# Optimization experiments

Hardware: AMD Instinct MI355X
Metric: run time of the kernel (lower is better)

The kernel has to match this reference:

```python
import jax, jax.numpy as jnp
import numpy as np

Z = 100000      # batch (edges)
MUL = 16        # multiplicity of Rs_in1 / Rs_out irreps
DW = MUL * 1 * MUL  # 256 weights per path (mul_1*mul_2*mul_out)
SQRT2 = 2.0 ** 0.5
SQRT3 = 3.0 ** 0.5
COUNT0 = 32.0 ** 0.5   # l=0 output: paths (0,0,0) and (1,1,0), 16+16 contributions
COUNT1 = 48.0 ** 0.5   # l=1 output: paths (0,1,1),(1,0,1),(1,1,1), 16*3 contributions


def setup_inputs() -> dict:
    key = jax.random.key(0)
    k1, k2, k3 = jax.random.split(key, 3)
    x1 = jax.random.normal(k1, (Z, 64), dtype=jnp.float32)    # [(16,0),(16,1)]
    x2 = jax.random.normal(k2, (Z, 4), dtype=jnp.float32)     # [(1,0),(1,1)]
    w = jax.random.normal(k3, (Z, 5 * DW), dtype=jnp.float32) # 5 paths x 256
    return {"x1": x1, "x2": x2, "w": w}


def reference(x1, x2, w):
    z = x1.shape[0]
    # slice inputs into irreps
    s1_0 = x1[:, :MUL]                          # (z, 16)        l=0
    s1_1 = x1[:, MUL:MUL + 3 * MUL].reshape(z, MUL, 3)  # (z, 16, 3)  l=1
    s2_0 = x2[:, :1]                            # (z, 1)         l=0
    s2_1 = x2[:, 1:4].reshape(z, 1, 3)          # (z, 1, 3)      l=1
    # per-path weights (z, u=16, v=1, w=16)
    sw0 = w[:, 0 * DW:1 * DW].reshape(z, MUL, 1, MUL)
    sw1 = w[:, 1 * DW:2 * DW].reshape(z, MUL, 1, MUL)
    sw2 = w[:, 2 * DW:3 * DW].reshape(z, MUL, 1, MUL)
    sw3 = w[:, 3 * DW:4 * DW].reshape(z, MUL, 1, MUL) / SQRT3
    sw4 = w[:, 4 * DW:5 * DW].reshape(z, MUL, 1, MUL) / SQRT2
    out0 = jnp.einsum('zuvw,zu,zv->zw', sw0, s1_0, s2_0)
    out1 = jnp.einsum('zuvw,zu,zvi->zwi', sw1, s1_0, s2_1)
    out1 = out1 + jnp.einsum('zuvw,zui,zv->zwi', sw2, s1_1, s2_0)
    out0 = out0 + jnp.einsum('zuvw,zui,zvi->zw', sw3, s1_1, s2_1)
    cross = jnp.cross(s1_1[:, :, None, :], s2_1[:, None, :, :], axis=3)  # (z,16,1,3)
    out1 = out1 + jnp.einsum('zuvw,zuvi->zwi', sw4, cross)
    # count normalization
    out0 = out0 / COUNT0                        # (z, 16)
    out1 = (out1 / COUNT1).reshape(z, 3 * MUL)  # (z, 48)
    return jnp.concatenate([out0, out1], axis=1)  # (z, 64)
```

## Files before the change

kernel.cpp:

```cpp
#include <hip/hip_runtime.h>


__global__ __launch_bounds__(256, 4) void ctp_kernel(
    const float* __restrict__ x1,
    const float* __restrict__ x2,
    const float* __restrict__ w,
    float* __restrict__ out,
    int Z)
{
    const int lane = threadIdx.x & 63;
    const int wid  = threadIdx.x >> 6;
    const int wavesPerBlock = blockDim.x >> 6;
    const int gwave  = blockIdx.x * wavesPerBlock + wid;
    const int nwaves = gridDim.x * wavesPerBlock;

    const int u = lane >> 2;
    const int c = lane & 3;

    const float inv32 = 0.17677669529663687f;
    const float inv48 = 0.14433756729740643f;
    const float inv3  = 0.57735026918962576f;
    const float inv2  = 0.70710678118654752f;

    for (int row = gwave; row < Z; row += nwaves) {
        const float* x1r = x1 + (size_t)row * 64;
        const float4 x2v = *(const float4*)(x2 + (size_t)row * 4);
        const float s20   = x2v.x;
        const float s21_0 = x2v.y, s21_1 = x2v.z, s21_2 = x2v.w;

        const float s10   = x1r[u];
        const float s11_0 = x1r[16 + 3*u + 0];
        const float s11_1 = x1r[16 + 3*u + 1];
        const float s11_2 = x1r[16 + 3*u + 2];

        const float4* wr = (const float4*)(w + (size_t)row * 1280);
        const float4 w0 = wr[lane];
        const float4 w1 = wr[ 64 + lane];
        const float4 w2 = wr[128 + lane];
        const float4 w3 = wr[192 + lane];
        const float4 w4 = wr[256 + lane];

        const float ka  = s10 * s20 * inv32;
        const float kd  = (s11_0*s21_0 + s11_1*s21_1 + s11_2*s21_2) * (inv3 * inv32);
        const float kb0 = s10 * s21_0 * inv48;
        const float kb1 = s10 * s21_1 * inv48;
        const float kb2 = s10 * s21_2 * inv48;
        const float kc0 = s11_0 * s20 * inv48;
        const float kc1 = s11_1 * s20 * inv48;
        const float kc2 = s11_2 * s20 * inv48;
        const float sc  = inv2 * inv48;
        const float ke0 = (s11_1*s21_2 - s11_2*s21_1) * sc;
        const float ke1 = (s11_2*s21_0 - s11_0*s21_2) * sc;
        const float ke2 = (s11_0*s21_1 - s11_1*s21_0) * sc;

        const float w0a[4] = {w0.x, w0.y, w0.z, w0.w};
        const float w1a[4] = {w1.x, w1.y, w1.z, w1.w};
        const float w2a[4] = {w2.x, w2.y, w2.z, w2.w};
        const float w3a[4] = {w3.x, w3.y, w3.z, w3.w};
        const float w4a[4] = {w4.x, w4.y, w4.z, w4.w};

        float acc0[4];
        float acc1[4][3];
        #pragma unroll
        for (int j = 0; j < 4; ++j) {
            acc0[j] = w0a[j] * ka + w3a[j] * kd;
            acc1[j][0] = w1a[j] * kb0 + w2a[j] * kc0 + w4a[j] * ke0;
            acc1[j][1] = w1a[j] * kb1 + w2a[j] * kc1 + w4a[j] * ke1;
            acc1[j][2] = w1a[j] * kb2 + w2a[j] * kc2 + w4a[j] * ke2;
        }

        #pragma unroll
        for (int m = 4; m <= 32; m <<= 1) {
            #pragma unroll
            for (int j = 0; j < 4; ++j) {
                acc0[j]    += __shfl_xor(acc0[j],    m, 64);
                acc1[j][0] += __shfl_xor(acc1[j][0], m, 64);
                acc1[j][1] += __shfl_xor(acc1[j][1], m, 64);
                acc1[j][2] += __shfl_xor(acc1[j][2], m, 64);
            }
        }

        float* outr = out + (size_t)row * 64;
        if (lane < 4) {
            *(float4*)(outr + 4*c) = make_float4(acc0[0], acc0[1], acc0[2], acc0[3]);
        } else if (lane < 16) {
            const int t = (lane >> 2) - 1;
            float v0, v1, v2, v3;
            if (t == 0)      { v0 = acc1[0][0]; v1 = acc1[0][1]; v2 = acc1[0][2]; v3 = acc1[1][0]; }
            else if (t == 1) { v0 = acc1[1][1]; v1 = acc1[1][2]; v2 = acc1[2][0]; v3 = acc1[2][1]; }
            else             { v0 = acc1[2][2]; v1 = acc1[3][0]; v2 = acc1[3][1]; v3 = acc1[3][2]; }
            *(float4*)(outr + 16 + 12*c + 4*t) = make_float4(v0, v1, v2, v3);
        }
    }
}

extern "C" void kernel_launch(void* const* d_in, const int* in_sizes, int n_in,
                              void* d_out, int out_size, void* d_ws, size_t ws_size,
                              hipStream_t stream) {
    const float* x1 = (const float*)d_in[0];
    const float* x2 = (const float*)d_in[1];
    const float* w  = (const float*)d_in[2];
    float* out = (float*)d_out;

    const int Z = in_sizes[1] / 4;

    const int blocks = 2048;
    hipLaunchKernelGGL(ctp_kernel, dim3(blocks), dim3(256), 0, stream,
                       x1, x2, w, out, Z);
}
```

Before: 657.6 us.

## Software-pipeline row loads, use halving shuffle reduction and nontemporal accesses

Each wave now prefetches the next row's weights and inputs into registers while it computes the current row, so load latency overlaps with compute. The butterfly reduction changes to a recursive-halving scheme: each stage exchanges half the remaining values, which cuts the shuffle count from 64 to 15, and every lane ends up writing one output scalar. Loads and stores use nontemporal hints because the streamed data is not reused. In exchange, register pressure roughly doubles for the prefetched data, and the kernel is likely memory-bandwidth bound anyway.

```diff
diff --git a/kernel.cpp b/kernel.cpp
--- a/kernel.cpp
+++ b/kernel.cpp
@@ -1,5 +1,7 @@
 #include <hip/hip_runtime.h>
 
+
+typedef float f32x4 __attribute__((ext_vector_type(4)));
 
 __global__ __launch_bounds__(256, 4) void ctp_kernel(
     const float* __restrict__ x1,
@@ -10,9 +12,8 @@
 {
     const int lane = threadIdx.x & 63;
     const int wid  = threadIdx.x >> 6;
-    const int wavesPerBlock = blockDim.x >> 6;
-    const int gwave  = blockIdx.x * wavesPerBlock + wid;
-    const int nwaves = gridDim.x * wavesPerBlock;
+    const int gwave  = blockIdx.x * (blockDim.x >> 6) + wid;
+    const int nwaves = gridDim.x * (blockDim.x >> 6);
 
     const int u = lane >> 2;
     const int c = lane & 3;
@@ -22,23 +23,52 @@
     const float inv3  = 0.57735026918962576f;
     const float inv2  = 0.70710678118654752f;
 
-    for (int row = gwave; row < Z; row += nwaves) {
+    const int off = (u < 4) ? (4*c + u) : (12*c + 12 + u);
+    const int ub0 = u & 1, ub1 = (u >> 1) & 1, ub2 = (u >> 2) & 1, ub3 = (u >> 3) & 1;
+
+    int row = gwave;
+    if (row >= Z) return;
+
+    f32x4 cw0, cw1, cw2, cw3, cw4, cx2;
+    float cxa, cxb, cxc, cxd;
+    {
+        const f32x4* wr = (const f32x4*)(w + (size_t)row * 1280);
+        cw0 = __builtin_nontemporal_load(wr + lane);
+        cw1 = __builtin_nontemporal_load(wr + 64 + lane);
+        cw2 = __builtin_nontemporal_load(wr + 128 + lane);
+        cw3 = __builtin_nontemporal_load(wr + 192 + lane);
+        cw4 = __builtin_nontemporal_load(wr + 256 + lane);
         const float* x1r = x1 + (size_t)row * 64;
-        const float4 x2v = *(const float4*)(x2 + (size_t)row * 4);
-        const float s20   = x2v.x;
-        const float s21_0 = x2v.y, s21_1 = x2v.z, s21_2 = x2v.w;
+        cxa = __builtin_nontemporal_load(x1r + u);
+        cxb = __builtin_nontemporal_load(x1r + 16 + 3*u);
+        cxc = __builtin_nontemporal_load(x1r + 17 + 3*u);
+        cxd = __builtin_nontemporal_load(x1r + 18 + 3*u);
+        cx2 = __builtin_nontemporal_load((const f32x4*)(x2 + (size_t)row * 4));
+    }
 
-        const float s10   = x1r[u];
-        const float s11_0 = x1r[16 + 3*u + 0];
-        const float s11_1 = x1r[16 + 3*u + 1];
-        const float s11_2 = x1r[16 + 3*u + 2];
+    while (true) {
+        const int nrow = row + nwaves;
+        const bool have_next = (nrow < Z);
 
-        const float4* wr = (const float4*)(w + (size_t)row * 1280);
-        const float4 w0 = wr[lane];
-        const float4 w1 = wr[ 64 + lane];
-        const float4 w2 = wr[128 + lane];
-        const float4 w3 = wr[192 + lane];
-        const float4 w4 = wr[256 + lane];
+        f32x4 nw0, nw1, nw2, nw3, nw4, nx2;
+        float nxa, nxb, nxc, nxd;
+        if (have_next) {
+            const f32x4* wr = (const f32x4*)(w + (size_t)nrow * 1280);
+            nw0 = __builtin_nontemporal_load(wr + lane);
+            nw1 = __builtin_nontemporal_load(wr + 64 + lane);
+            nw2 = __builtin_nontemporal_load(wr + 128 + lane);
+            nw3 = __builtin_nontemporal_load(wr + 192 + lane);
+            nw4 = __builtin_nontemporal_load(wr + 256 + lane);
+            const float* x1r = x1 + (size_t)nrow * 64;
+            nxa = __builtin_nontemporal_load(x1r + u);
+            nxb = __builtin_nontemporal_load(x1r + 16 + 3*u);
+            nxc = __builtin_nontemporal_load(x1r + 17 + 3*u);
+            nxd = __builtin_nontemporal_load(x1r + 18 + 3*u);
+            nx2 = __builtin_nontemporal_load((const f32x4*)(x2 + (size_t)nrow * 4));
+        }
+
+        const float s20 = cx2.x, s21_0 = cx2.y, s21_1 = cx2.z, s21_2 = cx2.w;
+        const float s10 = cxa, s11_0 = cxb, s11_1 = cxc, s11_2 = cxd;
 
         const float ka  = s10 * s20 * inv32;
         const float kd  = (s11_0*s21_0 + s11_1*s21_1 + s11_2*s21_2) * (inv3 * inv32);
@@ -53,44 +83,47 @@
         const float ke1 = (s11_2*s21_0 - s11_0*s21_2) * sc;
         const float ke2 = (s11_0*s21_1 - s11_1*s21_0) * sc;
 
-        const float w0a[4] = {w0.x, w0.y, w0.z, w0.w};
-        const float w1a[4] = {w1.x, w1.y, w1.z, w1.w};
-        const float w2a[4] = {w2.x, w2.y, w2.z, w2.w};
-        const float w3a[4] = {w3.x, w3.y, w3.z, w3.w};
-        const float w4a[4] = {w4.x, w4.y, w4.z, w4.w};
-
-        float acc0[4];
-        float acc1[4][3];
+        float v[16];
         #pragma unroll
         for (int j = 0; j < 4; ++j) {
-            acc0[j] = w0a[j] * ka + w3a[j] * kd;
-            acc1[j][0] = w1a[j] * kb0 + w2a[j] * kc0 + w4a[j] * ke0;
-            acc1[j][1] = w1a[j] * kb1 + w2a[j] * kc1 + w4a[j] * ke1;
-            acc1[j][2] = w1a[j] * kb2 + w2a[j] * kc2 + w4a[j] * ke2;
+            v[j]         = cw0[j]*ka  + cw3[j]*kd;
+            v[4 + 3*j+0] = cw1[j]*kb0 + cw2[j]*kc0 + cw4[j]*ke0;
+            v[4 + 3*j+1] = cw1[j]*kb1 + cw2[j]*kc1 + cw4[j]*ke1;
+            v[4 + 3*j+2] = cw1[j]*kb2 + cw2[j]*kc2 + cw4[j]*ke2;
         }
 
+        float a[8];
         #pragma unroll
-        for (int m = 4; m <= 32; m <<= 1) {
-            #pragma unroll
-            for (int j = 0; j < 4; ++j) {
-                acc0[j]    += __shfl_xor(acc0[j],    m, 64);
-                acc1[j][0] += __shfl_xor(acc1[j][0], m, 64);
-                acc1[j][1] += __shfl_xor(acc1[j][1], m, 64);
-                acc1[j][2] += __shfl_xor(acc1[j][2], m, 64);
-            }
+        for (int m = 0; m < 8; ++m) {
+            const float keep = ub0 ? v[2*m+1] : v[2*m];
+            const float send = ub0 ? v[2*m]   : v[2*m+1];
+            a[m] = keep + __shfl_xor(send, 4, 64);
+        }
+        float b[4];
+        #pragma unroll
+        for (int m = 0; m < 4; ++m) {
+            const float keep = ub1 ? a[2*m+1] : a[2*m];
+            const float send = ub1 ? a[2*m]   : a[2*m+1];
+            b[m] = keep + __shfl_xor(send, 8, 64);
+        }
+        float e[2];
+        #pragma unroll
+        for (int m = 0; m < 2; ++m) {
+            const float keep = ub2 ? b[2*m+1] : b[2*m];
+            const float send = ub2 ? b[2*m]   : b[2*m+1];
+            e[m] = keep + __shfl_xor(send, 16, 64);
+        }
+        {
+            const float keep = ub3 ? e[1] : e[0];
+            const float send = ub3 ? e[0] : e[1];
+            const float d = keep + __shfl_xor(send, 32, 64);
+            __builtin_nontemporal_store(d, out + (size_t)row * 64 + off);
         }
 
-        float* outr = out + (size_t)row * 64;
-        if (lane < 4) {
-            *(float4*)(outr + 4*c) = make_float4(acc0[0], acc0[1], acc0[2], acc0[3]);
-        } else if (lane < 16) {
-            const int t = (lane >> 2) - 1;
-            float v0, v1, v2, v3;
-            if (t == 0)      { v0 = acc1[0][0]; v1 = acc1[0][1]; v2 = acc1[0][2]; v3 = acc1[1][0]; }
-            else if (t == 1) { v0 = acc1[1][1]; v1 = acc1[1][2]; v2 = acc1[2][0]; v3 = acc1[2][1]; }
-            else             { v0 = acc1[2][2]; v1 = acc1[3][0]; v2 = acc1[3][1]; v3 = acc1[3][2]; }
-            *(float4*)(outr + 16 + 12*c + 4*t) = make_float4(v0, v1, v2, v3);
-        }
+        if (!have_next) break;
+        cw0 = nw0; cw1 = nw1; cw2 = nw2; cw3 = nw3; cw4 = nw4;
+        cxa = nxa; cxb = nxb; cxc = nxc; cxd = nxd; cx2 = nx2;
+        row = nrow;
     }
 }
 
@@ -104,7 +137,6 @@
 
     const int Z = in_sizes[1] / 4;
 
-    const int blocks = 2048;
-    hipLaunchKernelGGL(ctp_kernel, dim3(blocks), dim3(256), 0, stream,
+    hipLaunchKernelGGL(ctp_kernel, dim3(2048), dim3(256), 0, stream,
                        x1, x2, w, out, Z);
 }
```

Result: no change. 649.7 us (-1.2%).
